# Performance work log

Hardware: AMD Instinct MI355X
Metric: run time of the kernel (lower is better)

Reference implementation:

```python
import jax, jax.numpy as jnp
import numpy as np

B, S, IN, OUT, GS = 4, 2048, 4096, 16384, 32
G = IN // GS  # 128 groups per row


def setup_inputs() -> dict:
    key = jax.random.key(0)
    kx, ks, ki = jax.random.split(key, 3)
    x = jax.random.normal(kx, (B, S, IN), dtype=jnp.float32)
    # n_bits=2 initial codebook from the module
    codebook = jnp.array([-1.0, -0.25, 0.25, 1.0], dtype=jnp.float32)
    # scale is the log of per-group max-abs (use_exp_for_scale=True)
    scale = jax.random.normal(ks, (OUT, G, 1), dtype=jnp.float32) * 0.1 - 2.0
    indexes = jax.random.randint(ki, (OUT, G, GS), 0, 4, dtype=jnp.int32)
    return {"x": x, "codebook": codebook, "scale": scale, "indexes": indexes}


def reference(x, codebook, scale, indexes):
    # dequantize_weight: normalize codebook, gather per-element, exp-scale per group
    cb_norm = codebook / jnp.clip(jnp.max(jnp.abs(codebook)), 1e-8, None)
    w = cb_norm[indexes] * jnp.exp(scale)          # (OUT, G, GS)
    w = w.reshape(OUT, IN)                         # (OUT, IN)
    # F.linear(x, w) = x @ w.T
    return jnp.einsum("bsi,oi->bso", x, w)
```

## Files before the change

### kernel.cpp

```cpp
#include <hip/hip_runtime.h>
#include <stdint.h>


typedef unsigned short u16;
typedef __attribute__((ext_vector_type(8))) __bf16 bf16x8;
typedef __attribute__((ext_vector_type(4))) float f32x4;

__device__ __forceinline__ uint32_t f2bf(float f) {
  uint32_t u = __builtin_bit_cast(uint32_t, f);
  return (u + 0x7FFFu + ((u >> 16) & 1u)) >> 16;
}

__device__ __forceinline__ void gload16(const u16* g, u16* l) {
  __builtin_amdgcn_global_load_lds(
      (__attribute__((address_space(1))) void*)(g),
      (__attribute__((address_space(3))) void*)(l), 16, 0, 0);
}

__device__ __forceinline__ uint32_t sel4(uint32_t b0, uint32_t b1, uint32_t b2,
                                         uint32_t b3, int q) {
  uint32_t lo = (q & 1) ? b1 : b0;
  uint32_t hi = (q & 1) ? b3 : b2;
  return (q & 2) ? hi : lo;
}

__global__ __launch_bounds__(256) void cvt_x(const float* __restrict__ x,
                                             u16* __restrict__ xb, int n8) {
  int t = blockIdx.x * 256 + threadIdx.x;
  if (t >= n8) return;
  const float4* xp = reinterpret_cast<const float4*>(x) + (size_t)t * 2;
  float4 v0 = xp[0], v1 = xp[1];
  uint4 o;
  o.x = f2bf(v0.x) | (f2bf(v0.y) << 16);
  o.y = f2bf(v0.z) | (f2bf(v0.w) << 16);
  o.z = f2bf(v1.x) | (f2bf(v1.y) << 16);
  o.w = f2bf(v1.z) | (f2bf(v1.w) << 16);
  reinterpret_cast<uint4*>(xb)[t] = o;
}

__global__ __launch_bounds__(256) void dequant_w(
    const float* __restrict__ cb, const float* __restrict__ scale,
    const int* __restrict__ idx, u16* __restrict__ w, int ngroups) {
  int t = blockIdx.x * 256 + threadIdx.x;
  if (t >= ngroups) return;
  float m = fmaxf(fmaxf(fabsf(cb[0]), fabsf(cb[1])),
                  fmaxf(fabsf(cb[2]), fabsf(cb[3])));
  m = fmaxf(m, 1e-8f);
  float s = expf(scale[t]) / m;
  uint32_t b0 = f2bf(cb[0] * s), b1 = f2bf(cb[1] * s);
  uint32_t b2 = f2bf(cb[2] * s), b3 = f2bf(cb[3] * s);
  const int4* ip = reinterpret_cast<const int4*>(idx) + (size_t)t * 8;
  uint4* op = reinterpret_cast<uint4*>(w) + (size_t)t * 4;
#pragma unroll
  for (int v = 0; v < 4; ++v) {
    int4 qa = ip[v * 2], qb = ip[v * 2 + 1];
    uint4 o;
    o.x = sel4(b0, b1, b2, b3, qa.x) | (sel4(b0, b1, b2, b3, qa.y) << 16);
    o.y = sel4(b0, b1, b2, b3, qa.z) | (sel4(b0, b1, b2, b3, qa.w) << 16);
    o.z = sel4(b0, b1, b2, b3, qb.x) | (sel4(b0, b1, b2, b3, qb.y) << 16);
    o.w = sel4(b0, b1, b2, b3, qb.z) | (sel4(b0, b1, b2, b3, qb.w) << 16);
    op[v] = o;
  }
}

#define BM 256
#define BN 256
#define BK 64

__device__ __forceinline__ void memfence() { asm volatile("" ::: "memory"); }
__device__ __forceinline__ void BARx() {
  memfence();
  __builtin_amdgcn_s_barrier();
  memfence();
}

__global__ void __launch_bounds__(512, 2) gemm256(
    const u16* __restrict__ A, const u16* __restrict__ Bt,
    float* __restrict__ C, int M, int N, int K) {
  __shared__ u16 sm[2][2][BM * BK];

  const int nwg = gridDim.x;
  const int cpx = nwg >> 3;
  const int bid = blockIdx.x;
  const int swz = (bid & 7) * cpx + (bid >> 3);
  const int ntn = N / BN;
  const int m0 = (swz / ntn) * BM;
  const int n0 = (swz % ntn) * BN;

  const int tid = threadIdx.x;
  const int lane = tid & 63;
  const int wid = tid >> 6;
  const int wr = wid >> 2;
  const int wc = wid & 3;

  const int srow = wid * 8 + (lane >> 3);
  const int scol = (((lane & 7) ^ ((lane >> 3) & 7)) << 3);
  const u16* gA = A + (size_t)(m0 + srow) * K + scol;
  const u16* gB = Bt + (size_t)(n0 + srow) * K + scol;

#define STAGE(b, op, h, gp, kc)                                   \
  {                                                               \
    u16* d = &sm[(b)][(op)][(h)*8192 + wid * 512];                \
    const u16* g = (gp) + (size_t)((h)*128) * K + (kc);           \
    gload16(g, d);                                                \
    gload16(g + (size_t)64 * K, d + 4096);                        \
  }

  const int swzp0 = (((lane >> 4) ^ (lane & 7)) << 3);
  const int swzp1 = ((((lane >> 4) + 4) ^ (lane & 7)) << 3);
  const int lr = lane & 15;
  const int rAbase = (wr * 64 + lr) * BK;
  const int rBbase = (wc * 32 + lr) * BK;

  bf16x8 af[4][2], bv0[2][2], bv1[2][2];

#define LOADA(b, q)                                               \
  {                                                               \
    const u16* p = &sm[(b)][0][rAbase + (q)*8192];                \
    af[0][0] = *(const bf16x8*)(p + swzp0);                       \
    af[0][1] = *(const bf16x8*)(p + swzp1);                       \
    af[1][0] = *(const bf16x8*)(p + 1024 + swzp0);                \
    af[1][1] = *(const bf16x8*)(p + 1024 + swzp1);                \
    af[2][0] = *(const bf16x8*)(p + 2048 + swzp0);                \
    af[2][1] = *(const bf16x8*)(p + 2048 + swzp1);                \
    af[3][0] = *(const bf16x8*)(p + 3072 + swzp0);                \
    af[3][1] = *(const bf16x8*)(p + 3072 + swzp1);                \
  }
#define LOADBX(BV, b, pp)                                         \
  {                                                               \
    const u16* p = &sm[(b)][1][rBbase + (pp)*8192];               \
    BV[0][0] = *(const bf16x8*)(p + swzp0);                       \
    BV[0][1] = *(const bf16x8*)(p + swzp1);                       \
    BV[1][0] = *(const bf16x8*)(p + 1024 + swzp0);                \
    BV[1][1] = *(const bf16x8*)(p + 1024 + swzp1);                \
  }
#define MFMAQ(q, pp, BV)                                                    \
  {                                                                         \
    __builtin_amdgcn_s_setprio(1);                                          \
    _Pragma("unroll") for (int i = 0; i < 4; ++i)                           \
        _Pragma("unroll") for (int j = 0; j < 2; ++j)                       \
            _Pragma("unroll") for (int ks = 0; ks < 2; ++ks)                \
                acc[(q)*4 + i][(pp)*2 + j] =                                \
        __builtin_amdgcn_mfma_f32_16x16x32_bf16(                            \
            af[i][ks], BV[j][ks], acc[(q)*4 + i][(pp)*2 + j], 0, 0, 0);     \
    __builtin_amdgcn_s_setprio(0);                                          \
  }
#define VM6 asm volatile("s_waitcnt vmcnt(6)" ::: "memory");
#define VM0 asm volatile("s_waitcnt vmcnt(0)" ::: "memory");

  f32x4 acc[8][4];
#pragma unroll
  for (int i = 0; i < 8; ++i)
#pragma unroll
    for (int j = 0; j < 4; ++j) acc[i][j] = f32x4{0.f, 0.f, 0.f, 0.f};

  STAGE(0, 0, 0, gA, (size_t)0)
  STAGE(0, 1, 0, gB, (size_t)0)
  STAGE(0, 1, 1, gB, (size_t)0)
  STAGE(0, 0, 1, gA, (size_t)0)
  STAGE(1, 0, 0, gA, (size_t)64)
  STAGE(1, 1, 0, gB, (size_t)64)
  STAGE(1, 1, 1, gB, (size_t)64)
  VM6
  BARx();

#pragma unroll 1
  for (int i = 0; i < 31; ++i) {
    const size_t cT1 = (size_t)(2 * i + 1) * 64;
    const size_t cT2 = (size_t)(2 * i + 2) * 64;
    const size_t cT3 = (size_t)(2 * i + 3) * 64;
    LOADA(0, 0) LOADBX(bv0, 0, 0) LOADBX(bv1, 0, 1)
    STAGE(1, 0, 1, gA, cT1)
    BARx(); MFMAQ(0, 0, bv0)
    BARx(); MFMAQ(0, 1, bv1)
    LOADA(0, 1)
    STAGE(0, 0, 0, gA, cT2) STAGE(0, 1, 0, gB, cT2)
    BARx(); MFMAQ(1, 1, bv1)
    STAGE(0, 1, 1, gB, cT2)
    VM6
    BARx(); MFMAQ(1, 0, bv0)
    LOADA(1, 0) LOADBX(bv0, 1, 0) LOADBX(bv1, 1, 1)
    STAGE(0, 0, 1, gA, cT2)
    BARx(); MFMAQ(0, 0, bv0)
    BARx(); MFMAQ(0, 1, bv1)
    LOADA(1, 1)
    STAGE(1, 0, 0, gA, cT3) STAGE(1, 1, 0, gB, cT3)
    BARx(); MFMAQ(1, 1, bv1)
    STAGE(1, 1, 1, gB, cT3)
    VM6
    BARx(); MFMAQ(1, 0, bv0)
  }

  {
    const size_t cT1 = (size_t)63 * 64;
    LOADA(0, 0) LOADBX(bv0, 0, 0) LOADBX(bv1, 0, 1)
    STAGE(1, 0, 1, gA, cT1)
    BARx(); MFMAQ(0, 0, bv0)
    BARx(); MFMAQ(0, 1, bv1)
    LOADA(0, 1)
    BARx(); MFMAQ(1, 1, bv1)
    VM0
    BARx(); MFMAQ(1, 0, bv0)
    LOADA(1, 0) LOADBX(bv0, 1, 0) LOADBX(bv1, 1, 1)
    BARx(); MFMAQ(0, 0, bv0)
    BARx(); MFMAQ(0, 1, bv1)
    LOADA(1, 1)
    BARx(); MFMAQ(1, 1, bv1)
    BARx(); MFMAQ(1, 0, bv0)
  }

  const int crow0 = m0 + wr * 64 + ((lane >> 4) << 2);
  const int ccol0 = n0 + wc * 32 + (lane & 15);
#pragma unroll
  for (int q = 0; q < 2; ++q)
#pragma unroll
    for (int mi = 0; mi < 4; ++mi)
#pragma unroll
      for (int r = 0; r < 4; ++r) {
        float* cp = C + (size_t)(crow0 + q * 128 + mi * 16 + r) * N + ccol0;
#pragma unroll
        for (int pp = 0; pp < 2; ++pp)
#pragma unroll
          for (int j = 0; j < 2; ++j)
            cp[pp * 128 + j * 16] = acc[q * 4 + mi][pp * 2 + j][r];
      }
}

extern "C" void kernel_launch(void* const* d_in, const int* in_sizes, int n_in,
                              void* d_out, int out_size, void* d_ws,
                              size_t ws_size, hipStream_t stream) {
  const float* x = (const float*)d_in[0];
  const float* cb = (const float*)d_in[1];
  const float* scale = (const float*)d_in[2];
  const int* idx = (const int*)d_in[3];
  float* out = (float*)d_out;

  constexpr int M = 4 * 2048;
  constexpr int N = 16384;
  constexpr int K = 4096;

  u16* xb = (u16*)d_ws;
  u16* wb = xb + (size_t)M * K;

  const int n8 = M * K / 8;
  cvt_x<<<dim3(n8 / 256), dim3(256), 0, stream>>>(x, xb, n8);
  const int ngroups = N * (K / 32);
  dequant_w<<<dim3(ngroups / 256), dim3(256), 0, stream>>>(cb, scale, idx, wb,
                                                           ngroups);
  gemm256<<<dim3((M / BM) * (N / BN)), dim3(512), 0, stream>>>(xb, wb, out, M,
                                                               N, K);
}
```

Before: 1.038 ms.

## Double-buffer LDS fragment registers to overlap LDS reads with MFMA

Splits the A and B register fragments into two sets (afA/afB, bvX/bvY) and reorders the main loop so the next fragments are read from LDS while MFMAs on the current fragments are still running. The first fragments are preloaded before the loop, and the loads for the next half-tile move ahead of the barrier. The goal is to hide LDS read latency behind matrix-core work. The cost is more live vector registers, which can lower occupancy. Some LDS reads now come before a barrier, so they depend on the vmcnt wait for the data to be there.

```diff
diff --git a/kernel.cpp b/kernel.cpp
--- a/kernel.cpp
+++ b/kernel.cpp
@@ -112,19 +112,19 @@
   const int rAbase = (wr * 64 + lr) * BK;
   const int rBbase = (wc * 32 + lr) * BK;
 
-  bf16x8 af[4][2], bv0[2][2], bv1[2][2];
-
-#define LOADA(b, q)                                               \
+  bf16x8 afA[4][2], afB[4][2], bvX[2][2], bvY[2][2];
+
+#define LOADAX(AF, b, q)                                          \
   {                                                               \
     const u16* p = &sm[(b)][0][rAbase + (q)*8192];                \
-    af[0][0] = *(const bf16x8*)(p + swzp0);                       \
-    af[0][1] = *(const bf16x8*)(p + swzp1);                       \
-    af[1][0] = *(const bf16x8*)(p + 1024 + swzp0);                \
-    af[1][1] = *(const bf16x8*)(p + 1024 + swzp1);                \
-    af[2][0] = *(const bf16x8*)(p + 2048 + swzp0);                \
-    af[2][1] = *(const bf16x8*)(p + 2048 + swzp1);                \
-    af[3][0] = *(const bf16x8*)(p + 3072 + swzp0);                \
-    af[3][1] = *(const bf16x8*)(p + 3072 + swzp1);                \
+    AF[0][0] = *(const bf16x8*)(p + swzp0);                       \
+    AF[0][1] = *(const bf16x8*)(p + swzp1);                       \
+    AF[1][0] = *(const bf16x8*)(p + 1024 + swzp0);                \
+    AF[1][1] = *(const bf16x8*)(p + 1024 + swzp1);                \
+    AF[2][0] = *(const bf16x8*)(p + 2048 + swzp0);                \
+    AF[2][1] = *(const bf16x8*)(p + 2048 + swzp1);                \
+    AF[3][0] = *(const bf16x8*)(p + 3072 + swzp0);                \
+    AF[3][1] = *(const bf16x8*)(p + 3072 + swzp1);                \
   }
 #define LOADBX(BV, b, pp)                                         \
   {                                                               \
@@ -134,7 +134,7 @@
     BV[1][0] = *(const bf16x8*)(p + 1024 + swzp0);                \
     BV[1][1] = *(const bf16x8*)(p + 1024 + swzp1);                \
   }
-#define MFMAQ(q, pp, BV)                                                    \
+#define MFMAQ(q, pp, AF, BV)                                                \
   {                                                                         \
     __builtin_amdgcn_s_setprio(1);                                          \
     _Pragma("unroll") for (int i = 0; i < 4; ++i)                           \
@@ -142,7 +142,7 @@
             _Pragma("unroll") for (int ks = 0; ks < 2; ++ks)                \
                 acc[(q)*4 + i][(pp)*2 + j] =                                \
         __builtin_amdgcn_mfma_f32_16x16x32_bf16(                            \
-            af[i][ks], BV[j][ks], acc[(q)*4 + i][(pp)*2 + j], 0, 0, 0);     \
+            AF[i][ks], BV[j][ks], acc[(q)*4 + i][(pp)*2 + j], 0, 0, 0);     \
     __builtin_amdgcn_s_setprio(0);                                          \
   }
 #define VM6 asm volatile("s_waitcnt vmcnt(6)" ::: "memory");
@@ -163,50 +163,58 @@
   STAGE(1, 1, 1, gB, (size_t)64)
   VM6
   BARx();
+  LOADAX(afA, 0, 0)
+  LOADBX(bvX, 0, 0)
 
 #pragma unroll 1
   for (int i = 0; i < 31; ++i) {
     const size_t cT1 = (size_t)(2 * i + 1) * 64;
     const size_t cT2 = (size_t)(2 * i + 2) * 64;
     const size_t cT3 = (size_t)(2 * i + 3) * 64;
-    LOADA(0, 0) LOADBX(bv0, 0, 0) LOADBX(bv1, 0, 1)
+    LOADBX(bvY, 0, 1)
     STAGE(1, 0, 1, gA, cT1)
-    BARx(); MFMAQ(0, 0, bv0)
-    BARx(); MFMAQ(0, 1, bv1)
-    LOADA(0, 1)
+    BARx(); MFMAQ(0, 0, afA, bvX)
+    LOADAX(afB, 0, 1)
+    BARx(); MFMAQ(0, 1, afA, bvY)
     STAGE(0, 0, 0, gA, cT2) STAGE(0, 1, 0, gB, cT2)
-    BARx(); MFMAQ(1, 1, bv1)
+    BARx(); MFMAQ(1, 1, afB, bvY)
     STAGE(0, 1, 1, gB, cT2)
     VM6
-    BARx(); MFMAQ(1, 0, bv0)
-    LOADA(1, 0) LOADBX(bv0, 1, 0) LOADBX(bv1, 1, 1)
+    LOADAX(afA, 1, 0)
+    LOADBX(bvY, 1, 0)
+    BARx(); MFMAQ(1, 0, afB, bvX)
+    LOADBX(bvX, 1, 1)
     STAGE(0, 0, 1, gA, cT2)
-    BARx(); MFMAQ(0, 0, bv0)
-    BARx(); MFMAQ(0, 1, bv1)
-    LOADA(1, 1)
+    BARx(); MFMAQ(0, 0, afA, bvY)
+    LOADAX(afB, 1, 1)
+    BARx(); MFMAQ(0, 1, afA, bvX)
     STAGE(1, 0, 0, gA, cT3) STAGE(1, 1, 0, gB, cT3)
-    BARx(); MFMAQ(1, 1, bv1)
+    BARx(); MFMAQ(1, 1, afB, bvX)
     STAGE(1, 1, 1, gB, cT3)
     VM6
-    BARx(); MFMAQ(1, 0, bv0)
+    LOADAX(afA, 0, 0)
+    LOADBX(bvX, 0, 0)
+    BARx(); MFMAQ(1, 0, afB, bvY)
   }
 
   {
     const size_t cT1 = (size_t)63 * 64;
-    LOADA(0, 0) LOADBX(bv0, 0, 0) LOADBX(bv1, 0, 1)
+    LOADBX(bvY, 0, 1)
     STAGE(1, 0, 1, gA, cT1)
-    BARx(); MFMAQ(0, 0, bv0)
-    BARx(); MFMAQ(0, 1, bv1)
-    LOADA(0, 1)
-    BARx(); MFMAQ(1, 1, bv1)
+    BARx(); MFMAQ(0, 0, afA, bvX)
+    LOADAX(afB, 0, 1)
+    BARx(); MFMAQ(0, 1, afA, bvY)
+    BARx(); MFMAQ(1, 1, afB, bvY)
     VM0
-    BARx(); MFMAQ(1, 0, bv0)
-    LOADA(1, 0) LOADBX(bv0, 1, 0) LOADBX(bv1, 1, 1)
-    BARx(); MFMAQ(0, 0, bv0)
-    BARx(); MFMAQ(0, 1, bv1)
-    LOADA(1, 1)
-    BARx(); MFMAQ(1, 1, bv1)
-    BARx(); MFMAQ(1, 0, bv0)
+    LOADAX(afA, 1, 0)
+    LOADBX(bvY, 1, 0)
+    BARx(); MFMAQ(1, 0, afB, bvX)
+    LOADBX(bvX, 1, 1)
+    BARx(); MFMAQ(0, 0, afA, bvY)
+    LOADAX(afB, 1, 1)
+    BARx(); MFMAQ(0, 1, afA, bvX)
+    BARx(); MFMAQ(1, 1, afB, bvX)
+    BARx(); MFMAQ(1, 0, afB, bvY)
   }
 
   const int crow0 = m0 + wr * 64 + ((lane >> 4) << 2);
```

After: 2.708 ms. 161% more time.

## Restructure GEMM main loop into four phases with fewer barriers

Applied to the files above, without the earlier changes.

Reworks the double-buffered LDS pipeline in the bf16 MFMA GEMM main loop. The prologue now stages only the first K-tile, and the next tile's loads are issued inside the loop. Instead of eight barrier-separated MFMA quarters per iteration, there are four phases, each running two MFMA quarters after one barrier, with vmcnt waits placed to match. The aim is to cut barrier and synchronisation overhead per K step. The cost is a shorter prefetch distance, which could expose global-load latency and risk LDS buffer reuse hazards.

```diff
diff --git a/kernel.cpp b/kernel.cpp
--- a/kernel.cpp
+++ b/kernel.cpp
@@ -145,8 +145,7 @@
             af[i][ks], BV[j][ks], acc[(q)*4 + i][(pp)*2 + j], 0, 0, 0);     \
     __builtin_amdgcn_s_setprio(0);                                          \
   }
-#define VM6 asm volatile("s_waitcnt vmcnt(6)" ::: "memory");
-#define VM0 asm volatile("s_waitcnt vmcnt(0)" ::: "memory");
+#define VMW(n) asm volatile("s_waitcnt vmcnt(" #n ")" ::: "memory");
 
   f32x4 acc[8][4];
 #pragma unroll
@@ -158,55 +157,46 @@
   STAGE(0, 1, 0, gB, (size_t)0)
   STAGE(0, 1, 1, gB, (size_t)0)
   STAGE(0, 0, 1, gA, (size_t)0)
-  STAGE(1, 0, 0, gA, (size_t)64)
-  STAGE(1, 1, 0, gB, (size_t)64)
-  STAGE(1, 1, 1, gB, (size_t)64)
-  VM6
+  VMW(2)
   BARx();
 
 #pragma unroll 1
   for (int i = 0; i < 31; ++i) {
     const size_t cT1 = (size_t)(2 * i + 1) * 64;
     const size_t cT2 = (size_t)(2 * i + 2) * 64;
-    const size_t cT3 = (size_t)(2 * i + 3) * 64;
     LOADA(0, 0) LOADBX(bv0, 0, 0) LOADBX(bv1, 0, 1)
+    STAGE(1, 0, 0, gA, cT1) STAGE(1, 1, 0, gB, cT1) STAGE(1, 1, 1, gB, cT1)
+    VMW(6)
+    BARx(); MFMAQ(0, 0, bv0) MFMAQ(0, 1, bv1)
+    LOADA(0, 1)
     STAGE(1, 0, 1, gA, cT1)
-    BARx(); MFMAQ(0, 0, bv0)
-    BARx(); MFMAQ(0, 1, bv1)
-    LOADA(0, 1)
-    STAGE(0, 0, 0, gA, cT2) STAGE(0, 1, 0, gB, cT2)
-    BARx(); MFMAQ(1, 1, bv1)
-    STAGE(0, 1, 1, gB, cT2)
-    VM6
-    BARx(); MFMAQ(1, 0, bv0)
+    VMW(2)
+    BARx(); MFMAQ(1, 1, bv1) MFMAQ(1, 0, bv0)
     LOADA(1, 0) LOADBX(bv0, 1, 0) LOADBX(bv1, 1, 1)
+    STAGE(0, 0, 0, gA, cT2) STAGE(0, 1, 0, gB, cT2) STAGE(0, 1, 1, gB, cT2)
+    VMW(6)
+    BARx(); MFMAQ(0, 0, bv0) MFMAQ(0, 1, bv1)
+    LOADA(1, 1)
     STAGE(0, 0, 1, gA, cT2)
-    BARx(); MFMAQ(0, 0, bv0)
-    BARx(); MFMAQ(0, 1, bv1)
-    LOADA(1, 1)
-    STAGE(1, 0, 0, gA, cT3) STAGE(1, 1, 0, gB, cT3)
-    BARx(); MFMAQ(1, 1, bv1)
-    STAGE(1, 1, 1, gB, cT3)
-    VM6
-    BARx(); MFMAQ(1, 0, bv0)
+    VMW(2)
+    BARx(); MFMAQ(1, 1, bv1) MFMAQ(1, 0, bv0)
   }
 
   {
     const size_t cT1 = (size_t)63 * 64;
     LOADA(0, 0) LOADBX(bv0, 0, 0) LOADBX(bv1, 0, 1)
+    STAGE(1, 0, 0, gA, cT1) STAGE(1, 1, 0, gB, cT1) STAGE(1, 1, 1, gB, cT1)
+    VMW(6)
+    BARx(); MFMAQ(0, 0, bv0) MFMAQ(0, 1, bv1)
+    LOADA(0, 1)
     STAGE(1, 0, 1, gA, cT1)
-    BARx(); MFMAQ(0, 0, bv0)
-    BARx(); MFMAQ(0, 1, bv1)
-    LOADA(0, 1)
-    BARx(); MFMAQ(1, 1, bv1)
-    VM0
-    BARx(); MFMAQ(1, 0, bv0)
+    VMW(2)
+    BARx(); MFMAQ(1, 1, bv1) MFMAQ(1, 0, bv0)
     LOADA(1, 0) LOADBX(bv0, 1, 0) LOADBX(bv1, 1, 1)
-    BARx(); MFMAQ(0, 0, bv0)
-    BARx(); MFMAQ(0, 1, bv1)
+    VMW(0)
+    BARx(); MFMAQ(0, 0, bv0) MFMAQ(0, 1, bv1)
     LOADA(1, 1)
-    BARx(); MFMAQ(1, 1, bv1)
-    BARx(); MFMAQ(1, 0, bv0)
+    BARx(); MFMAQ(1, 1, bv1) MFMAQ(1, 0, bv0)
   }
 
   const int crow0 = m0 + wr * 64 + ((lane >> 4) << 2);
```

After: 1.081 ms. 1.04x slower.
